# Performance work log

Hardware: AMD Instinct MI355X
Metric: run time of the kernel (lower is better)

The kernel has to match this reference:

```python
import jax, jax.numpy as jnp
import numpy as np

B, Q, S, D, H = 8, 100, 4096, 256, 8
HD = D // H
EPS = 1e-5


def layer_norm(x, g, b):
    mu = jnp.mean(x, axis=-1, keepdims=True)
    var = jnp.mean(jnp.square(x - mu), axis=-1, keepdims=True)
    return (x - mu) * jax.lax.rsqrt(var + EPS) * g + b


def mha(q_in, k_in, v_in, w_in, b_in, w_out, b_out, bias=None):
    # torch nn.MultiheadAttention math (batch_first, dropout=0)
    wq, wk, wv = jnp.split(w_in, 3, axis=0)
    bq, bk, bv = jnp.split(b_in, 3, axis=0)
    Bq, Lq, _ = q_in.shape
    Lk = k_in.shape[1]
    q = (q_in @ wq.T + bq).reshape(Bq, Lq, H, HD)
    k = (k_in @ wk.T + bk).reshape(Bq, Lk, H, HD)
    v = (v_in @ wv.T + bv).reshape(Bq, Lk, H, HD)
    scores = jnp.einsum('bqhd,bkhd->bhqk', q, k) / jnp.sqrt(jnp.asarray(HD, q.dtype))
    if bias is not None:
        scores = scores + bias  # [B,1,Q,S] broadcast over heads (same per head)
    attn = jax.nn.softmax(scores, axis=-1)
    out = jnp.einsum('bhqk,bkhd->bqhd', attn, v).reshape(Bq, Lq, D)
    return out @ w_out.T + b_out


def setup_inputs() -> dict:
    key = jax.random.key(0)
    ks = jax.random.split(key, 12)
    s = 0.02
    return {
        'queries': jax.random.normal(ks[0], (B, Q, D), jnp.float32),
        'pixel_feat': jax.random.normal(ks[1], (B, S, D), jnp.float32),
        'prev_mask': jax.random.normal(ks[2], (B, Q, S), jnp.float32),
        'cross_in_w': jax.random.normal(ks[3], (3 * D, D), jnp.float32) * s,
        'cross_in_b': jnp.zeros((3 * D,), jnp.float32),
        'cross_out_w': jax.random.normal(ks[4], (D, D), jnp.float32) * s,
        'cross_out_b': jnp.zeros((D,), jnp.float32),
        'self_in_w': jax.random.normal(ks[5], (3 * D, D), jnp.float32) * s,
        'self_in_b': jnp.zeros((3 * D,), jnp.float32),
        'self_out_w': jax.random.normal(ks[6], (D, D), jnp.float32) * s,
        'self_out_b': jnp.zeros((D,), jnp.float32),
        'ln_cross_g': jnp.ones((D,), jnp.float32),
        'ln_cross_b': jnp.zeros((D,), jnp.float32),
        'ln_self_g': jnp.ones((D,), jnp.float32),
        'ln_self_b': jnp.zeros((D,), jnp.float32),
        'ln_ffn_g': jnp.ones((D,), jnp.float32),
        'ln_ffn_b': jnp.zeros((D,), jnp.float32),
        'ffn_w1': jax.random.normal(ks[7], (4 * D, D), jnp.float32) * s,
        'ffn_b1': jnp.zeros((4 * D,), jnp.float32),
        'ffn_w2': jax.random.normal(ks[8], (D, 4 * D), jnp.float32) * s,
        'ffn_b2': jnp.zeros((D,), jnp.float32),
    }


def reference(queries, pixel_feat, prev_mask,
              cross_in_w, cross_in_b, cross_out_w, cross_out_b,
              self_in_w, self_in_b, self_out_w, self_out_b,
              ln_cross_g, ln_cross_b, ln_self_g, ln_self_b, ln_ffn_g, ln_ffn_b,
              ffn_w1, ffn_b1, ffn_w2, ffn_b2):
    # masked cross-attn bias (no-grad region in torch; boolean ops have no grad)
    region = jax.nn.sigmoid(prev_mask) > 0.5                    # [B,Q,S]
    any_pos = jnp.any(region, axis=-1, keepdims=True)
    region = jnp.where(any_pos, region, jnp.ones_like(region))
    bias = (~region).astype(queries.dtype) * -10000.0
    bias = bias[:, None, :, :]                                  # [B,1,Q,S]

    q_out = mha(layer_norm(queries, ln_cross_g, ln_cross_b), pixel_feat, pixel_feat,
                cross_in_w, cross_in_b, cross_out_w, cross_out_b, bias)
    queries = queries + q_out

    q_norm = layer_norm(queries, ln_self_g, ln_self_b)
    q_out = mha(q_norm, q_norm, q_norm, self_in_w, self_in_b, self_out_w, self_out_b)
    queries = queries + q_out

    h = layer_norm(queries, ln_ffn_g, ln_ffn_b)
    h = jax.nn.gelu(h @ ffn_w1.T + ffn_b1, approximate=False) @ ffn_w2.T + ffn_b2
    return queries + h
```

## Files before the change

kernel.cpp:

```cpp
#include <hip/hip_runtime.h>
#include <hip/hip_bf16.h>
#include <math.h>

#define BQ 100
#define SB 8
#define SS 4096
#define DD 256
#define HH 8
#define HDD 32
#define NSPLIT 4
#define SCHUNK (SS / NSPLIT)
#define MROWS 800

typedef __attribute__((ext_vector_type(8))) short bf16x8;
typedef __attribute__((ext_vector_type(4))) float f32x4;

__device__ inline unsigned short f2bf(float f) {
    union { float f; unsigned u; } v; v.f = f;
    unsigned r = v.u + 0x7fff + ((v.u >> 16) & 1);
    return (unsigned short)(r >> 16);
}

__device__ inline unsigned pkbf(float x, float y) {
    union { __hip_bfloat162 h; unsigned u; } c;
    c.h = __float22bfloat162_rn(make_float2(x, y));
    return c.u;
}

__device__ inline bf16x8 load_bf8(const float* p) {
    float4 a = *(const float4*)p;
    float4 b = *(const float4*)(p + 4);
    union { unsigned u[4]; bf16x8 v; } r;
    r.u[0] = pkbf(a.x, a.y); r.u[1] = pkbf(a.z, a.w);
    r.u[2] = pkbf(b.x, b.y); r.u[3] = pkbf(b.z, b.w);
    return r.v;
}

#define TM 128
#define TN 128
#define TK 32

#define WOFF_CW   0
#define WOFF_SIW  196608
#define WOFF_COW  393216
#define WOFF_SOW  458752
#define WOFF_F1   524288
#define WOFF_F2   786432
#define WTOT      1048576

__global__ __launch_bounds__(256) void wprep(
        const float* __restrict__ cw, const float* __restrict__ siw,
        const float* __restrict__ cow, const float* __restrict__ sow,
        const float* __restrict__ f1, const float* __restrict__ f2,
        const float* __restrict__ pix,
        unsigned short* __restrict__ o, unsigned short* __restrict__ abf) {
    int b = blockIdx.x;
    int t = threadIdx.x;
    if (b >= 512) {
        size_t off = (size_t)(b - 512) * 2048 + (size_t)t * 8;
        const float* p = pix + off;
        float4 a = *(const float4*)p;
        float4 c = *(const float4*)(p + 4);
        uint4 pk;
        pk.x = pkbf(a.x, a.y); pk.y = pkbf(a.z, a.w);
        pk.z = pkbf(c.x, c.y); pk.w = pkbf(c.z, c.w);
        *(uint4*)(abf + off) = pk;
        return;
    }
    const float* src; size_t so, doff;
    if (b < 96)       { src = cw;  so = (size_t)b * 2048;         doff = WOFF_CW; }
    else if (b < 192) { src = siw; so = (size_t)(b - 96) * 2048;  doff = WOFF_SIW; }
    else if (b < 224) { src = cow; so = (size_t)(b - 192) * 2048; doff = WOFF_COW; }
    else if (b < 256) { src = sow; so = (size_t)(b - 224) * 2048; doff = WOFF_SOW; }
    else if (b < 384) { src = f1;  so = (size_t)(b - 256) * 2048; doff = WOFF_F1; }
    else              { src = f2;  so = (size_t)(b - 384) * 2048; doff = WOFF_F2; }
    const float* p = src + so + (size_t)t * 8;
    float4 a = *(const float4*)p;
    float4 c = *(const float4*)(p + 4);
    uint4 pk;
    pk.x = pkbf(a.x, a.y); pk.y = pkbf(a.z, a.w);
    pk.z = pkbf(c.x, c.y); pk.w = pkbf(c.z, c.w);
    *(uint4*)(o + doff + so + (size_t)t * 8) = pk;
}

__global__ __launch_bounds__(256, 4) void stage1(
        const float* __restrict__ queries,
        const float* __restrict__ ln_g, const float* __restrict__ ln_b,
        const unsigned short* __restrict__ wbf,
        const float* __restrict__ cb,
        float* __restrict__ q_cross,
        const unsigned short* __restrict__ Abf,
        unsigned short* __restrict__ Kb, unsigned short* __restrict__ Vb,
        const float* __restrict__ mask, unsigned* __restrict__ Mbits) {
    __shared__ __align__(16) char smem[21504];
    const int bid = blockIdx.x;
    const int t = threadIdx.x;

    if (bid < 1024) {
        const unsigned short* Wb = wbf + (size_t)DD * DD;
        const float* bias = cb + DD;
        int xcd = bid & 7, idx = bid >> 3;
        int mt = xcd + 8 * (idx >> 2);
        int ntl = idx & 3;
        int m0 = mt * TM, n0 = ntl * TN;
        int wave = t / 64, lane = t % 64;
        int wm = (wave % 2) * 64, wn = (wave / 2) * 64;
        int fr = lane % 16, quad = lane / 16;
        f32x4 acc[4][4] = {};

        const unsigned short* Ap = Abf + (size_t)(m0 + wm + fr) * DD + quad * 8;
        const unsigned short* Wp = Wb + (size_t)(n0 + wn + fr) * DD + quad * 8;

#pragma unroll
        for (int k0 = 0; k0 < DD; k0 += TK) {
            bf16x8 af[4], bv[4];
#pragma unroll
            for (int mi = 0; mi < 4; mi++)
                af[mi] = *(const bf16x8*)(Ap + (size_t)mi * 16 * DD + k0);
#pragma unroll
            for (int ni = 0; ni < 4; ni++)
                bv[ni] = *(const bf16x8*)(Wp + (size_t)ni * 16 * DD + k0);
#pragma unroll
            for (int mi = 0; mi < 4; mi++) {
                acc[mi][0] = __builtin_amdgcn_mfma_f32_16x16x32_bf16(af[mi], bv[0], acc[mi][0], 0, 0, 0);
                acc[mi][1] = __builtin_amdgcn_mfma_f32_16x16x32_bf16(af[mi], bv[1], acc[mi][1], 0, 0, 0);
                acc[mi][2] = __builtin_amdgcn_mfma_f32_16x16x32_bf16(af[mi], bv[2], acc[mi][2], 0, 0, 0);
                acc[mi][3] = __builtin_amdgcn_mfma_f32_16x16x32_bf16(af[mi], bv[3], acc[mi][3], 0, 0, 0);
            }
        }
#pragma unroll
        for (int ni = 0; ni < 4; ni++) {
            int n = n0 + wn + ni * 16 + fr;
            float bv = bias[n];
            unsigned short* dst = (n < 256) ? Kb : Vb;
            int hh = (n >> 5) & 7, d = n & 31;
#pragma unroll
            for (int mi = 0; mi < 4; mi++) {
#pragma unroll
                for (int r = 0; r < 4; r++) {
                    int m = m0 + wm + mi * 16 + quad * 4 + r;
                    int bb = m >> 12, s = m & (SS - 1);
                    dst[((((size_t)bb * HH + hh) * SS + s) << 5) + d] =
                        f2bf(acc[mi][ni][r] + bv);
                }
            }
        }
    } else if (bid < 1824) {
        int row = bid - 1024;
        unsigned* words = (unsigned*)smem;
        unsigned* orred = (unsigned*)(smem + 512);
        int w = t >> 6, lane = t & 63;
        const float* mp = mask + (size_t)row * SS + lane;
        float mv[16];
#pragma unroll
        for (int i = 0; i < 16; i++) mv[i] = mp[(w * 16 + i) * 64];
        unsigned lor = 0;
#pragma unroll
        for (int i = 0; i < 16; i++) {
            unsigned long long bal = __ballot(mv[i] > 0.f);
            if (lane == 0) {
                words[(w * 16 + i) * 2] = (unsigned)bal;
                words[(w * 16 + i) * 2 + 1] = (unsigned)(bal >> 32);
            }
            lor |= (unsigned)(bal | (bal >> 32));
        }
        if (lane == 0) orred[w] = lor;
        __syncthreads();
        unsigned anyv = orred[0] | orred[1] | orred[2] | orred[3];
        if (t < 128) Mbits[(size_t)row * 128 + t] = anyv ? words[t] : 0xFFFFFFFFu;
    } else {
        typedef unsigned short (*arow_t)[264];
        arow_t Aq = (arow_t)smem;
        float* mu_s = (float*)(smem + 16896);
        float* rs_s = mu_s + 32;
        float (*prt)[8][2] = (float(*)[8][2])(rs_s + 32);
        int idx = bid - 1824;
        int nq = idx & 1, my = idx >> 1;
        int m0 = my * 32;
        int row = t & 31, cs = t >> 5;
        const float* xp = queries + (size_t)(m0 + row) * DD + cs * 32;
        float s = 0.f, ss = 0.f;
#pragma unroll
        for (int c = 0; c < 32; c += 4) {
            float4 v = *(const float4*)(xp + c);
            s += v.x + v.y + v.z + v.w;
            ss += v.x * v.x + v.y * v.y + v.z * v.z + v.w * v.w;
        }
        prt[row][cs][0] = s; prt[row][cs][1] = ss;
        __syncthreads();
        if (t < 32) {
            float sum = 0.f, sq = 0.f;
#pragma unroll
            for (int k = 0; k < 8; k++) { sum += prt[t][k][0]; sq += prt[t][k][1]; }
            float mu = sum * (1.0f / DD);
            float var = sq * (1.0f / DD) - mu * mu;
            mu_s[t] = mu;
            rs_s[t] = rsqrtf(var + 1e-5f);
        }
        __syncthreads();
        {
            float mu = mu_s[row], r = rs_s[row];
            int col0 = cs * 32;
#pragma unroll
            for (int c = 0; c < 32; c += 8) {
                int col = col0 + c;
                float4 v0 = *(const float4*)(xp + c);
                float4 v1 = *(const float4*)(xp + c + 4);
                float4 g0 = *(const float4*)(ln_g + col);
                float4 g1 = *(const float4*)(ln_g + col + 4);
                float4 b0 = *(const float4*)(ln_b + col);
                float4 b1 = *(const float4*)(ln_b + col + 4);
                uint4 pk;
                pk.x = pkbf((v0.x - mu) * r * g0.x + b0.x, (v0.y - mu) * r * g0.y + b0.y);
                pk.y = pkbf((v0.z - mu) * r * g0.z + b0.z, (v0.w - mu) * r * g0.w + b0.w);
                pk.z = pkbf((v1.x - mu) * r * g1.x + b1.x, (v1.y - mu) * r * g1.y + b1.y);
                pk.w = pkbf((v1.z - mu) * r * g1.z + b1.z, (v1.w - mu) * r * g1.w + b1.w);
                *(uint4*)&Aq[row][col] = pk;
            }
        }
        __syncthreads();
        int w = t >> 6, lane = t & 63;
        int fr = lane & 15, quad = lane >> 4;
        int n0 = nq * 128 + w * 32;
        f32x4 acc[2][2] = {};
        const unsigned short* Wq0 = wbf + (size_t)(n0 + fr) * DD + quad * 8;
        const unsigned short* Wq1 = Wq0 + (size_t)16 * DD;
#pragma unroll
        for (int k0 = 0; k0 < DD; k0 += 32) {
            bf16x8 a0 = *(const bf16x8*)&Aq[fr][k0 + quad * 8];
            bf16x8 a1 = *(const bf16x8*)&Aq[16 + fr][k0 + quad * 8];
            bf16x8 w0 = *(const bf16x8*)(Wq0 + k0);
            bf16x8 w1 = *(const bf16x8*)(Wq1 + k0);
            acc[0][0] = __builtin_amdgcn_mfma_f32_16x16x32_bf16(a0, w0, acc[0][0], 0, 0, 0);
            acc[0][1] = __builtin_amdgcn_mfma_f32_16x16x32_bf16(a0, w1, acc[0][1], 0, 0, 0);
            acc[1][0] = __builtin_amdgcn_mfma_f32_16x16x32_bf16(a1, w0, acc[1][0], 0, 0, 0);
            acc[1][1] = __builtin_amdgcn_mfma_f32_16x16x32_bf16(a1, w1, acc[1][1], 0, 0, 0);
        }
#pragma unroll
        for (int ni = 0; ni < 2; ni++) {
            int n = n0 + ni * 16 + fr;
            float bv = cb[n];
#pragma unroll
            for (int mi = 0; mi < 2; mi++) {
#pragma unroll
                for (int r = 0; r < 4; r++) {
                    int m = m0 + mi * 16 + quad * 4 + r;
                    q_cross[(size_t)m * DD + n] = acc[mi][ni][r] + bv;
                }
            }
        }
    }
}

template<int MODE>
__global__ __launch_bounds__(64, 4) void ln_gemm(
        const float* __restrict__ X, const float* __restrict__ gam,
        const float* __restrict__ bet,
        const unsigned short* __restrict__ W, const float* __restrict__ bias,
        const float* __restrict__ res,
        float* __restrict__ C, int N) {
    __shared__ unsigned short As[32][264];
    __shared__ float mu_s[32], rs_s[32];
    __shared__ float prt[32][2][2];
    const int t = threadIdx.x;
    const int fr = t & 15, quad = t >> 4;
    const int m0 = blockIdx.y * 32, n0 = blockIdx.x * 32;
    const int row = t & 31, half = t >> 5;

    const float* xp = X + (size_t)(m0 + row) * DD + half * 128;
    float s = 0.f, ss = 0.f;
#pragma unroll
    for (int c = 0; c < 128; c += 4) {
        float4 v = *(const float4*)(xp + c);
        s += v.x + v.y + v.z + v.w;
        ss += v.x * v.x + v.y * v.y + v.z * v.z + v.w * v.w;
    }
    prt[row][half][0] = s;
    prt[row][half][1] = ss;
    __syncthreads();
    if (t < 32) {
        float sum = prt[t][0][0] + prt[t][1][0];
        float sq  = prt[t][0][1] + prt[t][1][1];
        float mu = sum * (1.0f / DD);
        float var = sq * (1.0f / DD) - mu * mu;
        mu_s[t] = mu;
        rs_s[t] = rsqrtf(var + 1e-5f);
    }
    __syncthreads();
    {
        float mu = mu_s[row], r = rs_s[row];
#pragma unroll
        for (int c = 0; c < 128; c += 8) {
            int col = half * 128 + c;
            float4 v0 = *(const float4*)(xp + c);
            float4 v1 = *(const float4*)(xp + c + 4);
            float4 g0 = *(const float4*)(gam + col);
            float4 g1 = *(const float4*)(gam + col + 4);
            float4 b0 = *(const float4*)(bet + col);
            float4 b1 = *(const float4*)(bet + col + 4);
            uint4 pk;
            pk.x = pkbf((v0.x - mu) * r * g0.x + b0.x, (v0.y - mu) * r * g0.y + b0.y);
            pk.y = pkbf((v0.z - mu) * r * g0.z + b0.z, (v0.w - mu) * r * g0.w + b0.w);
            pk.z = pkbf((v1.x - mu) * r * g1.x + b1.x, (v1.y - mu) * r * g1.y + b1.y);
            pk.w = pkbf((v1.z - mu) * r * g1.z + b1.z, (v1.w - mu) * r * g1.w + b1.w);
            *(uint4*)&As[row][col] = pk;
        }
    }
    __syncthreads();

    f32x4 acc[2][2] = {};
    const unsigned short* Wp0 = W + (size_t)(n0 + fr) * DD + quad * 8;
    const unsigned short* Wp1 = Wp0 + (size_t)16 * DD;
#pragma unroll
    for (int k0 = 0; k0 < DD; k0 += 32) {
        bf16x8 a0 = *(const bf16x8*)&As[fr][k0 + quad * 8];
        bf16x8 a1 = *(const bf16x8*)&As[16 + fr][k0 + quad * 8];
        bf16x8 w0 = *(const bf16x8*)(Wp0 + k0);
        bf16x8 w1 = *(const bf16x8*)(Wp1 + k0);
        acc[0][0] = __builtin_amdgcn_mfma_f32_16x16x32_bf16(a0, w0, acc[0][0], 0, 0, 0);
        acc[0][1] = __builtin_amdgcn_mfma_f32_16x16x32_bf16(a0, w1, acc[0][1], 0, 0, 0);
        acc[1][0] = __builtin_amdgcn_mfma_f32_16x16x32_bf16(a1, w0, acc[1][0], 0, 0, 0);
        acc[1][1] = __builtin_amdgcn_mfma_f32_16x16x32_bf16(a1, w1, acc[1][1], 0, 0, 0);
    }

#pragma unroll
    for (int ni = 0; ni < 2; ni++) {
        int n = n0 + ni * 16 + fr;
        float bv = bias[n];
#pragma unroll
        for (int mi = 0; mi < 2; mi++) {
#pragma unroll
            for (int r = 0; r < 4; r++) {
                int m = m0 + mi * 16 + quad * 4 + r;
                float v = acc[mi][ni][r] + bv;
                if (MODE == 1) {
                    v = 0.5f * v * (1.0f + erff(v * 0.70710678118654752f));
                } else if (MODE == 2) {
                    v += res[(size_t)m * N + n];
                }
                C[(size_t)m * N + n] = v;
            }
        }
    }
}

__global__ __launch_bounds__(64, 4) void comb_gemm(
        const float* __restrict__ Opart, const float* __restrict__ mpart,
        const float* __restrict__ lpart,
        const unsigned short* __restrict__ W, const float* __restrict__ bias,
        const float* __restrict__ res,
        float* __restrict__ C) {
    __shared__ unsigned short As[32][264];
    const int t = threadIdx.x;
    const int fr = t & 15, quad = t >> 4;
    const int m0 = blockIdx.y * 32, n0 = blockIdx.x * 32;
    const int row = t & 31, half = t >> 5;

    {
        int m = m0 + row;
        int b = m / BQ, q = m % BQ;
#pragma unroll
        for (int h = half * 4; h < half * 4 + 4; h++) {
            float mv[NSPLIT], wsp[NSPLIT];
            float mstar = -1e30f;
#pragma unroll
            for (int sp = 0; sp < NSPLIT; sp++) {
                mv[sp] = mpart[((size_t)(b * NSPLIT + sp) * HH + h) * BQ + q];
                mstar = fmaxf(mstar, mv[sp]);
            }
            float lstar = 0.f;
#pragma unroll
            for (int sp = 0; sp < NSPLIT; sp++) {
                wsp[sp] = __expf(mv[sp] - mstar);
                lstar += lpart[((size_t)(b * NSPLIT + sp) * HH + h) * BQ + q] * wsp[sp];
            }
            float inv = 1.0f / lstar;
#pragma unroll
            for (int d = 0; d < HDD; d += 8) {
                float o[8] = {};
#pragma unroll
                for (int sp = 0; sp < NSPLIT; sp++) {
                    const float* op = Opart +
                        ((size_t)(b * NSPLIT + sp) * BQ + q) * DD + h * HDD + d;
                    float4 a = *(const float4*)op;
                    float4 b4 = *(const float4*)(op + 4);
                    o[0] += a.x * wsp[sp];  o[1] += a.y * wsp[sp];
                    o[2] += a.z * wsp[sp];  o[3] += a.w * wsp[sp];
                    o[4] += b4.x * wsp[sp]; o[5] += b4.y * wsp[sp];
                    o[6] += b4.z * wsp[sp]; o[7] += b4.w * wsp[sp];
                }
                uint4 pk;
                pk.x = pkbf(o[0] * inv, o[1] * inv);
                pk.y = pkbf(o[2] * inv, o[3] * inv);
                pk.z = pkbf(o[4] * inv, o[5] * inv);
                pk.w = pkbf(o[6] * inv, o[7] * inv);
                *(uint4*)&As[row][h * HDD + d] = pk;
            }
        }
    }
    __syncthreads();

    f32x4 acc[2][2] = {};
    const unsigned short* Wp0 = W + (size_t)(n0 + fr) * DD + quad * 8;
    const unsigned short* Wp1 = Wp0 + (size_t)16 * DD;
#pragma unroll
    for (int k0 = 0; k0 < DD; k0 += 32) {
        bf16x8 a0 = *(const bf16x8*)&As[fr][k0 + quad * 8];
        bf16x8 a1 = *(const bf16x8*)&As[16 + fr][k0 + quad * 8];
        bf16x8 w0 = *(const bf16x8*)(Wp0 + k0);
        bf16x8 w1 = *(const bf16x8*)(Wp1 + k0);
        acc[0][0] = __builtin_amdgcn_mfma_f32_16x16x32_bf16(a0, w0, acc[0][0], 0, 0, 0);
        acc[0][1] = __builtin_amdgcn_mfma_f32_16x16x32_bf16(a0, w1, acc[0][1], 0, 0, 0);
        acc[1][0] = __builtin_amdgcn_mfma_f32_16x16x32_bf16(a1, w0, acc[1][0], 0, 0, 0);
        acc[1][1] = __builtin_amdgcn_mfma_f32_16x16x32_bf16(a1, w1, acc[1][1], 0, 0, 0);
    }

#pragma unroll
    for (int ni = 0; ni < 2; ni++) {
        int n = n0 + ni * 16 + fr;
        float bv = bias[n];
#pragma unroll
        for (int mi = 0; mi < 2; mi++) {
#pragma unroll
            for (int r = 0; r < 4; r++) {
                int m = m0 + mi * 16 + quad * 4 + r;
                float v = acc[mi][ni][r] + bv + res[(size_t)m * DD + n];
                C[(size_t)m * DD + n] = v;
            }
        }
    }
}

template<int KK, int SPLITK, int MODE>
__global__ __launch_bounds__(64, 4) void gemm_skinny2(
        const float* __restrict__ A, const unsigned short* __restrict__ W,
        const float* __restrict__ bias, const float* __restrict__ res,
        float* __restrict__ C, float* __restrict__ Cp, int N) {
    const int lane = threadIdx.x;
    const int fr = lane & 15, quad = lane >> 4;
    const int m0 = blockIdx.y * 32;
    const int n0 = blockIdx.x * 32;
    const int sk = blockIdx.z;
    const int KCH = KK / SPLITK;

    f32x4 acc[2][2] = {};
    const float* Ap0 = A + (size_t)(m0 + fr) * KK + sk * KCH + quad * 8;
    const float* Ap1 = Ap0 + (size_t)16 * KK;
    const unsigned short* Wp0 = W + (size_t)(n0 + fr) * KK + sk * KCH + quad * 8;
    const unsigned short* Wp1 = Wp0 + (size_t)16 * KK;

#pragma unroll
    for (int k0 = 0; k0 < KCH; k0 += 32) {
        bf16x8 a0 = load_bf8(Ap0 + k0);
        bf16x8 a1 = load_bf8(Ap1 + k0);
        bf16x8 w0 = *(const bf16x8*)(Wp0 + k0);
        bf16x8 w1 = *(const bf16x8*)(Wp1 + k0);
        acc[0][0] = __builtin_amdgcn_mfma_f32_16x16x32_bf16(a0, w0, acc[0][0], 0, 0, 0);
        acc[0][1] = __builtin_amdgcn_mfma_f32_16x16x32_bf16(a0, w1, acc[0][1], 0, 0, 0);
        acc[1][0] = __builtin_amdgcn_mfma_f32_16x16x32_bf16(a1, w0, acc[1][0], 0, 0, 0);
        acc[1][1] = __builtin_amdgcn_mfma_f32_16x16x32_bf16(a1, w1, acc[1][1], 0, 0, 0);
    }

    if (SPLITK == 1) {
#pragma unroll
        for (int ni = 0; ni < 2; ni++) {
            int n = n0 + ni * 16 + fr;
            float bv = bias[n];
#pragma unroll
            for (int mi = 0; mi < 2; mi++) {
#pragma unroll
                for (int r = 0; r < 4; r++) {
                    int m = m0 + mi * 16 + quad * 4 + r;
                    float v = acc[mi][ni][r] + bv;
                    if (MODE == 1) {
                        v = 0.5f * v * (1.0f + erff(v * 0.70710678118654752f));
                    } else if (MODE == 2) {
                        v += res[(size_t)m * N + n];
                    }
                    C[(size_t)m * N + n] = v;
                }
            }
        }
    } else {
        float* dst = Cp + (size_t)sk * MROWS * N;
#pragma unroll
        for (int ni = 0; ni < 2; ni++) {
            int n = n0 + ni * 16 + fr;
#pragma unroll
            for (int mi = 0; mi < 2; mi++) {
#pragma unroll
                for (int r = 0; r < 4; r++) {
                    int m = m0 + mi * 16 + quad * 4 + r;
                    dst[(size_t)m * N + n] = acc[mi][ni][r];
                }
            }
        }
    }
}

template<int SPLITK, int MODE>
__global__ void gemm_combine(const float* __restrict__ Cp,
                             const float* __restrict__ bias,
                             const float* __restrict__ res,
                             float* __restrict__ C, int N) {
    int m = blockIdx.x;
    for (int n = threadIdx.x; n < N; n += 256) {
        float v = bias[n];
#pragma unroll
        for (int sk = 0; sk < SPLITK; sk++)
            v += Cp[((size_t)sk * MROWS + m) * N + n];
        if (MODE == 1) {
            v = 0.5f * v * (1.0f + erff(v * 0.70710678118654752f));
        } else if (MODE == 2) {
            v += res[(size_t)m * N + n];
        }
        C[(size_t)m * N + n] = v;
    }
}

#define QT 64
#define ST 128

__global__ __launch_bounds__(256) void cross_attn_mfma(
        const float* __restrict__ Qm,
        const unsigned short* __restrict__ Kb,
        const unsigned short* __restrict__ Vb,
        const unsigned* __restrict__ Mbits,
        float* __restrict__ Opart,
        float* __restrict__ mpart,
        float* __restrict__ lpart) {
    __shared__ unsigned short Qs[QT][40];
    __shared__ unsigned short Ks[ST][40];
    __shared__ unsigned short Vt[HDD][136];
    __shared__ unsigned short Ps[QT][136];
    __shared__ unsigned Mq[QT][4];
    __shared__ float red[QT][17];
    __shared__ float m_s[QT], alpha_s[QT], l_s[QT];

    const int qb = blockIdx.x, h = blockIdx.y;
    const int b = blockIdx.z / NSPLIT, sp = blockIdx.z % NSPLIT;
    const int t = threadIdx.x;
    const int w = t >> 6, lane = t & 63;
    const int fr = lane & 15, quad = lane >> 4;
    const int q0 = qb * QT;
    const int qlim = min(BQ - q0, QT);

    {
        int q = t >> 2, c0 = (t & 3) * 8;
        float4 v0 = make_float4(0.f, 0.f, 0.f, 0.f), v1 = v0;
        if (q < qlim) {
            const float* qp = Qm + (size_t)(b * BQ + q0 + q) * DD + h * HDD + c0;
            v0 = *(const float4*)qp;
            v1 = *(const float4*)(qp + 4);
        }
        const float sc = 0.17677669529663687f;
        uint4 pq;
        pq.x = pkbf(v0.x * sc, v0.y * sc);
        pq.y = pkbf(v0.z * sc, v0.w * sc);
        pq.z = pkbf(v1.x * sc, v1.y * sc);
        pq.w = pkbf(v1.z * sc, v1.w * sc);
        *(uint4*)&Qs[q][c0] = pq;
        if (t < QT) { m_s[t] = -1e30f; l_s[t] = 0.f; }
    }

    f32x4 oacc[2] = {};
    const unsigned short* Kbase = Kb + (((size_t)(b * HH + h)) * SS << 5);
    const unsigned short* Vbase = Vb + (((size_t)(b * HH + h)) * SS << 5);

    for (int s0 = sp * SCHUNK; s0 < (sp + 1) * SCHUNK; s0 += ST) {
        __syncthreads();
        {
            int r = t >> 1, half = t & 1;
            const unsigned short* kp = Kbase + ((size_t)(s0 + r) << 5) + half * 16;
            *(uint4*)&Ks[r][half * 16] = *(const uint4*)kp;
            *(uint4*)&Ks[r][half * 16 + 8] = *(const uint4*)(kp + 8);
            const unsigned short* vp = Vbase + ((size_t)(s0 + r) << 5) + half * 16;
            union { uint4 u; unsigned short s[8]; } v0, v1;
            v0.u = *(const uint4*)vp;
            v1.u = *(const uint4*)(vp + 8);
#pragma unroll
            for (int j = 0; j < 8; j++) Vt[half * 16 + j][r] = v0.s[j];
#pragma unroll
            for (int j = 0; j < 8; j++) Vt[half * 16 + 8 + j][r] = v1.s[j];
        }
        {
            int q = t >> 2, wd = t & 3;
            unsigned mword = 0xFFFFFFFFu;
            if (q < qlim)
                mword = Mbits[(size_t)(b * BQ + q0 + q) * 128 + (s0 >> 5) + wd];
            Mq[q][wd] = mword;
        }
        __syncthreads();

        bf16x8 af[2];
#pragma unroll
        for (int mt = 0; mt < 2; mt++)
            af[mt] = *(const bf16x8*)&Ks[w * 32 + mt * 16 + fr][quad * 8];
        f32x4 st[2][4];
#pragma unroll
        for (int nt = 0; nt < 4; nt++) {
            bf16x8 bq = *(const bf16x8*)&Qs[nt * 16 + fr][quad * 8];
#pragma unroll
            for (int mt = 0; mt < 2; mt++) {
                f32x4 z = {0.f, 0.f, 0.f, 0.f};
                st[mt][nt] = __builtin_amdgcn_mfma_f32_16x16x32_bf16(af[mt], bq, z, 0, 0, 0);
            }
        }

        float pmax[4] = {-1e30f, -1e30f, -1e30f, -1e30f};
#pragma unroll
        for (int nt = 0; nt < 4; nt++) {
            unsigned mword = Mq[nt * 16 + fr][w];
#pragma unroll
            for (int mt = 0; mt < 2; mt++)
#pragma unroll
                for (int r = 0; r < 4; r++) {
                    int bitpos = mt * 16 + quad * 4 + r;
                    float v = st[mt][nt][r];
                    if (!((mword >> bitpos) & 1u)) v -= 10000.f;
                    st[mt][nt][r] = v;
                    pmax[nt] = fmaxf(pmax[nt], v);
                }
        }
#pragma unroll
        for (int nt = 0; nt < 4; nt++)
            red[nt * 16 + fr][w * 4 + quad] = pmax[nt];
        __syncthreads();

        if (t < QT) {
            float mt_ = -1e30f;
#pragma unroll
            for (int k = 0; k < 16; k++) mt_ = fmaxf(mt_, red[t][k]);
            float mo = m_s[t], mn = fmaxf(mo, mt_);
            m_s[t] = mn;
            alpha_s[t] = __expf(mo - mn);
        }
        __syncthreads();

        float psum[4] = {0.f, 0.f, 0.f, 0.f};
#pragma unroll
        for (int nt = 0; nt < 4; nt++) {
            float mrow = m_s[nt * 16 + fr];
#pragma unroll
            for (int mt = 0; mt < 2; mt++) {
                float p0 = __expf(st[mt][nt][0] - mrow);
                float p1 = __expf(st[mt][nt][1] - mrow);
                float p2 = __expf(st[mt][nt][2] - mrow);
                float p3 = __expf(st[mt][nt][3] - mrow);
                psum[nt] += p0 + p1 + p2 + p3;
                uint2 pk;
                pk.x = pkbf(p0, p1);
                pk.y = pkbf(p2, p3);
                *(uint2*)&Ps[nt * 16 + fr][w * 32 + mt * 16 + quad * 4] = pk;
            }
        }
#pragma unroll
        for (int nt = 0; nt < 4; nt++)
            red[nt * 16 + fr][w * 4 + quad] = psum[nt];
        __syncthreads();

        if (t < QT) {
            float s = 0.f;
#pragma unroll
            for (int k = 0; k < 16; k++) s += red[t][k];
            l_s[t] = l_s[t] * alpha_s[t] + s;
        }

#pragma unroll
        for (int r = 0; r < 4; r++) {
            float a = alpha_s[w * 16 + quad * 4 + r];
            oacc[0][r] *= a; oacc[1][r] *= a;
        }
#pragma unroll
        for (int k0 = 0; k0 < ST; k0 += 32) {
            bf16x8 ap = *(const bf16x8*)&Ps[w * 16 + fr][k0 + quad * 8];
            bf16x8 bv0 = *(const bf16x8*)&Vt[fr][k0 + quad * 8];
            bf16x8 bv1 = *(const bf16x8*)&Vt[16 + fr][k0 + quad * 8];
            oacc[0] = __builtin_amdgcn_mfma_f32_16x16x32_bf16(ap, bv0, oacc[0], 0, 0, 0);
            oacc[1] = __builtin_amdgcn_mfma_f32_16x16x32_bf16(ap, bv1, oacc[1], 0, 0, 0);
        }
    }
    __syncthreads();

    int part = b * NSPLIT + sp;
    if (t < qlim) {
        mpart[((size_t)part * HH + h) * BQ + q0 + t] = m_s[t];
        lpart[((size_t)part * HH + h) * BQ + q0 + t] = l_s[t];
    }
#pragma unroll
    for (int nd = 0; nd < 2; nd++) {
#pragma unroll
        for (int r = 0; r < 4; r++) {
            int q = w * 16 + quad * 4 + r;
            if (q < qlim)
                Opart[((size_t)part * BQ + q0 + q) * DD + h * HDD + nd * 16 + fr] = oacc[nd][r];
        }
    }
}

__global__ void attn_kernel(const float* __restrict__ Qm, int sq, int qo0,
                            const float* __restrict__ Km, int sk, int ko0,
                            const float* __restrict__ Vm, int sv, int vo0,
                            float* __restrict__ Out, int so, int oo0,
                            int Slen, int Qlen, float scale) {
    int q = blockIdx.x, h = blockIdx.y, b = blockIdx.z;
    int tid = threadIdx.x;
    __shared__ float qv[32];
    __shared__ float sc[128];
    __shared__ float red[256];
    __shared__ float part[8][33];
    int qrow = b * Qlen + q;
    if (tid < 32) qv[tid] = Qm[(size_t)qrow * sq + qo0 + h * HDD + tid] * scale;
    __syncthreads();

    float lmax = -1e30f;
    for (int s = tid; s < Slen; s += 256) {
        const float* kp = Km + (size_t)(b * Slen + s) * sk + ko0 + h * HDD;
        float dot = 0.f;
#pragma unroll
        for (int d = 0; d < HDD; d += 4) {
            float4 k4 = *(const float4*)(kp + d);
            dot += qv[d] * k4.x + qv[d + 1] * k4.y + qv[d + 2] * k4.z + qv[d + 3] * k4.w;
        }
        sc[s] = dot;
        lmax = fmaxf(lmax, dot);
    }
    red[tid] = lmax; __syncthreads();
    for (int off = 128; off > 0; off >>= 1) {
        if (tid < off) red[tid] = fmaxf(red[tid], red[tid + off]);
        __syncthreads();
    }
    float m = red[0];
    __syncthreads();
    float lsum = 0.f;
    for (int s = tid; s < Slen; s += 256) {
        float e = __expf(sc[s] - m);
        sc[s] = e;
        lsum += e;
    }
    red[tid] = lsum; __syncthreads();
    for (int off = 128; off > 0; off >>= 1) {
        if (tid < off) red[tid] += red[tid + off];
        __syncthreads();
    }
    float inv = 1.0f / red[0];

    int d = tid & 31, g = tid >> 5;
    float acc = 0.f;
    for (int s = g; s < Slen; s += 8)
        acc += sc[s] * Vm[(size_t)(b * Slen + s) * sv + vo0 + h * HDD + d];
    part[g][d] = acc; __syncthreads();
    if (g == 0) {
        float t = 0.f;
#pragma unroll
        for (int gg = 0; gg < 8; gg++) t += part[gg][d];
        Out[(size_t)qrow * so + oo0 + h * HDD + d] = t * inv;
    }
}

extern "C" void kernel_launch(void* const* d_in, const int* in_sizes, int n_in,
                              void* d_out, int out_size, void* d_ws, size_t ws_size,
                              hipStream_t stream) {
    const float* queries    = (const float*)d_in[0];
    const float* pixel_feat = (const float*)d_in[1];
    const float* prev_mask  = (const float*)d_in[2];
    const float* cross_in_w  = (const float*)d_in[3];
    const float* cross_in_b  = (const float*)d_in[4];
    const float* cross_out_w = (const float*)d_in[5];
    const float* cross_out_b = (const float*)d_in[6];
    const float* self_in_w   = (const float*)d_in[7];
    const float* self_in_b   = (const float*)d_in[8];
    const float* self_out_w  = (const float*)d_in[9];
    const float* self_out_b  = (const float*)d_in[10];
    const float* ln_cross_g  = (const float*)d_in[11];
    const float* ln_cross_b  = (const float*)d_in[12];
    const float* ln_self_g   = (const float*)d_in[13];
    const float* ln_self_b   = (const float*)d_in[14];
    const float* ln_ffn_g    = (const float*)d_in[15];
    const float* ln_ffn_b    = (const float*)d_in[16];
    const float* ffn_w1 = (const float*)d_in[17];
    const float* ffn_b1 = (const float*)d_in[18];
    const float* ffn_w2 = (const float*)d_in[19];
    const float* ffn_b2 = (const float*)d_in[20];
    float* out = (float*)d_out;

    const int NQ = SB * BQ;
    const int NK = SB * SS;

    float* ws = (float*)d_ws;
    unsigned* Mbits = (unsigned*)ws;   ws += (size_t)NQ * 128;
    float* q_cross  = ws;              ws += (size_t)NQ * DD;
    unsigned short* Kbk = (unsigned short*)ws;
    ws += (size_t)NK * DD / 2;
    unsigned short* Vbk = (unsigned short*)ws;
    ws += (size_t)NK * DD / 2;
    float* queries1 = ws;              ws += (size_t)NQ * DD;
    float* qkv      = ws;              ws += (size_t)NQ * 3 * DD;
    float* attn2    = ws;              ws += (size_t)NQ * DD;
    float* queries2 = ws;              ws += (size_t)NQ * DD;
    float* ffn_h    = ws;              ws += (size_t)NQ * 4 * DD;
    float* Csplit   = ws;              ws += (size_t)4 * MROWS * DD;
    float* Opart    = ws;              ws += (size_t)SB * NSPLIT * BQ * DD;
    float* mpart    = ws;              ws += (size_t)SB * NSPLIT * HH * BQ;
    float* lpart    = ws;              ws += (size_t)SB * NSPLIT * HH * BQ;
    unsigned short* wbf = (unsigned short*)ws;
    ws += WTOT / 2;
    unsigned short* Abf = (unsigned short*)ws;

    const float scale = 0.17677669529663687f;

    wprep<<<4608, 256, 0, stream>>>(
        cross_in_w, self_in_w, cross_out_w, self_out_w, ffn_w1, ffn_w2,
        pixel_feat, wbf, Abf);

    stage1<<<1874, 256, 0, stream>>>(
        queries, ln_cross_g, ln_cross_b, wbf, cross_in_b, q_cross,
        Abf, Kbk, Vbk, prev_mask, Mbits);

    cross_attn_mfma<<<dim3(2, HH, SB * NSPLIT), 256, 0, stream>>>(
        q_cross, Kbk, Vbk, Mbits, Opart, mpart, lpart);
    comb_gemm<<<dim3(8, 25), 64, 0, stream>>>(
        Opart, mpart, lpart, wbf + WOFF_COW, cross_out_b, queries, queries1);

    ln_gemm<0><<<dim3(24, 25), 64, 0, stream>>>(
        queries1, ln_self_g, ln_self_b, wbf + WOFF_SIW, self_in_b, nullptr,
        qkv, 3 * DD);
    attn_kernel<<<dim3(BQ, HH, SB), 256, 0, stream>>>(
        qkv, 3 * DD, 0, qkv, 3 * DD, DD, qkv, 3 * DD, 2 * DD,
        attn2, DD, 0, BQ, BQ, scale);
    gemm_skinny2<256, 1, 2><<<dim3(8, 25), 64, 0, stream>>>(
        attn2, wbf + WOFF_SOW, self_out_b, queries1, queries2, nullptr, DD);

    ln_gemm<1><<<dim3(32, 25), 64, 0, stream>>>(
        queries2, ln_ffn_g, ln_ffn_b, wbf + WOFF_F1, ffn_b1, nullptr,
        ffn_h, 4 * DD);
    gemm_skinny2<1024, 4, 2><<<dim3(8, 25, 4), 64, 0, stream>>>(
        ffn_h, wbf + WOFF_F2, ffn_b2, nullptr, nullptr, Csplit, DD);
    gemm_combine<4, 2><<<MROWS, 256, 0, stream>>>(
        Csplit, ffn_b2, queries2, out, DD);
}
```

Before: 273.2 us.

## Stage K/V projection tiles through LDS with async global_load_lds and XOR swizzle

The K/V projection GEMM in stage1 used to load A and W fragments straight from global memory into registers for every wave. It now stages 128x64 bf16 tiles of A and W into shared memory with global_load_lds, using an XOR-swizzled column layout, and has waves read MFMA fragments from LDS. This is meant to cut redundant global traffic, since waves sharing rows or columns no longer each fetch them. In exchange it adds two barriers per K step with no double buffering, and the larger shared allocation lowers the occupancy hint from 4 to 3 blocks.

Result: faster. 253.9 us (-7.1%).

```diff
diff --git a/kernel.cpp b/kernel.cpp
--- a/kernel.cpp
+++ b/kernel.cpp
@@ -36,9 +36,14 @@
     return r.v;
 }
 
+typedef __attribute__((address_space(1))) const void gas_void;
+typedef __attribute__((address_space(3))) void las_void;
+__device__ inline void gl_lds16(const unsigned short* g, unsigned short* l) {
+    __builtin_amdgcn_global_load_lds((gas_void*)g, (las_void*)l, 16, 0, 0);
+}
+
 #define TM 128
 #define TN 128
-#define TK 32
 
 #define WOFF_CW   0
 #define WOFF_SIW  196608
@@ -83,7 +88,7 @@
     *(uint4*)(o + doff + so + (size_t)t * 8) = pk;
 }
 
-__global__ __launch_bounds__(256, 4) void stage1(
+__global__ __launch_bounds__(256, 3) void stage1(
         const float* __restrict__ queries,
         const float* __restrict__ ln_g, const float* __restrict__ ln_b,
         const unsigned short* __restrict__ wbf,
@@ -92,40 +97,64 @@
         const unsigned short* __restrict__ Abf,
         unsigned short* __restrict__ Kb, unsigned short* __restrict__ Vb,
         const float* __restrict__ mask, unsigned* __restrict__ Mbits) {
-    __shared__ __align__(16) char smem[21504];
+    __shared__ __align__(16) char smem[32768];
     const int bid = blockIdx.x;
     const int t = threadIdx.x;
 
     if (bid < 1024) {
+        unsigned short* As = (unsigned short*)smem;
+        unsigned short* Bs = As + 128 * 64;
         const unsigned short* Wb = wbf + (size_t)DD * DD;
         const float* bias = cb + DD;
         int xcd = bid & 7, idx = bid >> 3;
         int mt = xcd + 8 * (idx >> 2);
         int ntl = idx & 3;
         int m0 = mt * TM, n0 = ntl * TN;
-        int wave = t / 64, lane = t % 64;
-        int wm = (wave % 2) * 64, wn = (wave / 2) * 64;
-        int fr = lane % 16, quad = lane / 16;
+        int wave = t >> 6, lane = t & 63;
+        int wm = (wave & 1) * 64, wn = (wave >> 1) * 64;
+        int fr = lane & 15, quad = lane >> 4;
         f32x4 acc[4][4] = {};
 
-        const unsigned short* Ap = Abf + (size_t)(m0 + wm + fr) * DD + quad * 8;
-        const unsigned short* Wp = Wb + (size_t)(n0 + wn + fr) * DD + quad * 8;
-
-#pragma unroll
-        for (int k0 = 0; k0 < DD; k0 += TK) {
-            bf16x8 af[4], bv[4];
-#pragma unroll
-            for (int mi = 0; mi < 4; mi++)
-                af[mi] = *(const bf16x8*)(Ap + (size_t)mi * 16 * DD + k0);
-#pragma unroll
-            for (int ni = 0; ni < 4; ni++)
-                bv[ni] = *(const bf16x8*)(Wp + (size_t)ni * 16 * DD + k0);
-#pragma unroll
-            for (int mi = 0; mi < 4; mi++) {
-                acc[mi][0] = __builtin_amdgcn_mfma_f32_16x16x32_bf16(af[mi], bv[0], acc[mi][0], 0, 0, 0);
-                acc[mi][1] = __builtin_amdgcn_mfma_f32_16x16x32_bf16(af[mi], bv[1], acc[mi][1], 0, 0, 0);
-                acc[mi][2] = __builtin_amdgcn_mfma_f32_16x16x32_bf16(af[mi], bv[2], acc[mi][2], 0, 0, 0);
-                acc[mi][3] = __builtin_amdgcn_mfma_f32_16x16x32_bf16(af[mi], bv[3], acc[mi][3], 0, 0, 0);
+        int crow[4], ccol[4];
+#pragma unroll
+        for (int i = 0; i < 4; i++) {
+            int c = i * 256 + t;
+            crow[i] = c >> 3;
+            ccol[i] = (c & 7) ^ (crow[i] & 7);
+        }
+
+        for (int k0 = 0; k0 < DD; k0 += 64) {
+            __syncthreads();
+#pragma unroll
+            for (int i = 0; i < 4; i++) {
+                gl_lds16(Abf + (size_t)(m0 + crow[i]) * DD + k0 + ccol[i] * 8,
+                         As + (i * 256 + t) * 8);
+                gl_lds16(Wb + (size_t)(n0 + crow[i]) * DD + k0 + ccol[i] * 8,
+                         Bs + (i * 256 + t) * 8);
+            }
+            __syncthreads();
+#pragma unroll
+            for (int kk = 0; kk < 2; kk++) {
+                bf16x8 af[4], bv[4];
+#pragma unroll
+                for (int mi = 0; mi < 4; mi++) {
+                    int row = wm + mi * 16 + fr;
+                    int j = (kk * 4 + quad) ^ (row & 7);
+                    af[mi] = *(const bf16x8*)(As + row * 64 + j * 8);
+                }
+#pragma unroll
+                for (int ni = 0; ni < 4; ni++) {
+                    int row = wn + ni * 16 + fr;
+                    int j = (kk * 4 + quad) ^ (row & 7);
+                    bv[ni] = *(const bf16x8*)(Bs + row * 64 + j * 8);
+                }
+#pragma unroll
+                for (int mi = 0; mi < 4; mi++) {
+                    acc[mi][0] = __builtin_amdgcn_mfma_f32_16x16x32_bf16(af[mi], bv[0], acc[mi][0], 0, 0, 0);
+                    acc[mi][1] = __builtin_amdgcn_mfma_f32_16x16x32_bf16(af[mi], bv[1], acc[mi][1], 0, 0, 0);
+                    acc[mi][2] = __builtin_amdgcn_mfma_f32_16x16x32_bf16(af[mi], bv[2], acc[mi][2], 0, 0, 0);
+                    acc[mi][3] = __builtin_amdgcn_mfma_f32_16x16x32_bf16(af[mi], bv[3], acc[mi][3], 0, 0, 0);
+                }
             }
         }
 #pragma unroll
```
